# Kernel optimization log

Hardware: AMD Instinct MI355X
Metric: run time of the kernel (lower is better)

The kernel has to match this reference:

```python
import jax, jax.numpy as jnp
import numpy as np

NUM_JOINT = 19
BATCH = 262144
ROOT_SCALE = 200.0
# Topologically-ordered humanoid skeleton: parent[j] < j for all non-root joints.
# 0: hips, 1-4: spine/head chain, 5-8: left arm, 9-12: right arm, 13-15: left leg, 16-18: right leg
PARENTS = np.array([-1, 0, 1, 2, 3, 2, 5, 6, 7, 2, 9, 10, 11, 0, 13, 14, 0, 16, 17], dtype=np.int32)


def quaternion_to_matrix(q):
    # q: [..., 4] in (w, x, y, z) order (pytorch3d convention, non-unit tolerant)
    w, x, y, z = q[..., 0], q[..., 1], q[..., 2], q[..., 3]
    two_s = 2.0 / jnp.sum(q * q, axis=-1)
    r = jnp.stack([
        1.0 - two_s * (y * y + z * z), two_s * (x * y - z * w), two_s * (x * z + y * w),
        two_s * (x * y + z * w), 1.0 - two_s * (x * x + z * z), two_s * (y * z - x * w),
        two_s * (x * z - y * w), two_s * (y * z + x * w), 1.0 - two_s * (x * x + y * y),
    ], axis=-1)
    return r.reshape(q.shape[:-1] + (3, 3))


def setup_inputs() -> dict:
    key = jax.random.key(0)
    k1, k2, k3 = jax.random.split(key, 3)
    root_position = jax.random.normal(k1, (BATCH, 3), dtype=jnp.float32)
    joint = jax.random.normal(k2, (BATCH, NUM_JOINT * 4), dtype=jnp.float32)
    # Homogeneous translation matrices per bone: identity rotation, translation in column 3.
    trans = jax.random.normal(k3, (NUM_JOINT, 3), dtype=jnp.float32) * 10.0
    offsets = jnp.tile(jnp.eye(4, dtype=jnp.float32)[None], (NUM_JOINT, 1, 1))
    offsets = offsets.at[:, :3, 3].set(trans)
    return {"root_position": root_position, "joint": joint, "offsets": offsets}


def reference(root_position, joint, offsets):
    B = joint.shape[0]
    q = joint.reshape(B, NUM_JOINT, 4)
    R3 = quaternion_to_matrix(q)  # [B, J, 3, 3]
    R4 = jnp.zeros((B, NUM_JOINT, 4, 4), dtype=joint.dtype)
    R4 = R4.at[:, :, :3, :3].set(R3).at[:, :, 3, 3].set(1.0)
    # RT = rotation @ bone offset, batched over all joints at once
    RT = jnp.einsum('bjik,jkl->bjil', R4, offsets)  # [B, J, 4, 4]
    # Sequential parent-child chain over the (small, fixed) skeleton tree
    mats = [RT[:, 0]]
    for j in range(1, NUM_JOINT):
        mats.append(jnp.matmul(mats[PARENTS[j]], RT[:, j]))
    M = jnp.stack(mats, axis=1)  # [B, J, 4, 4] world transforms
    # joint position = column 3 of the homogeneous transform (== transpose row 3 in source)
    pos = M[:, :, :, 3]  # [B, J, 4]
    pos = pos.at[:, :, :3].add((root_position * ROOT_SCALE)[:, None, :])
    return pos
```

## Files before the change

kernel.cpp:

```cpp
#include <hip/hip_runtime.h>
#include <stdint.h>

#define NJ 19
#define ROOT_SCALE 200.0f
#define BLOCK 64
#define ROWF 76
#define ROWV 19

struct Xform { float r[9]; float t[3]; };

__device__ __forceinline__ void quat_rt(float w, float x, float y, float z,
                                        float tx, float ty, float tz, Xform& o) {
    float ts = 2.0f / (w*w + x*x + y*y + z*z);
    o.r[0] = 1.0f - ts*(y*y + z*z); o.r[1] = ts*(x*y - z*w);        o.r[2] = ts*(x*z + y*w);
    o.r[3] = ts*(x*y + z*w);        o.r[4] = 1.0f - ts*(x*x + z*z); o.r[5] = ts*(y*z - x*w);
    o.r[6] = ts*(x*z - y*w);        o.r[7] = ts*(y*z + x*w);        o.r[8] = 1.0f - ts*(x*x + y*y);
    o.t[0] = o.r[0]*tx + o.r[1]*ty + o.r[2]*tz;
    o.t[1] = o.r[3]*tx + o.r[4]*ty + o.r[5]*tz;
    o.t[2] = o.r[6]*tx + o.r[7]*ty + o.r[8]*tz;
}

__device__ __forceinline__ void compose(const Xform& p, const Xform& l, Xform& o) {
#pragma unroll
    for (int i = 0; i < 3; ++i) {
        o.r[i*3+0] = p.r[i*3+0]*l.r[0] + p.r[i*3+1]*l.r[3] + p.r[i*3+2]*l.r[6];
        o.r[i*3+1] = p.r[i*3+0]*l.r[1] + p.r[i*3+1]*l.r[4] + p.r[i*3+2]*l.r[7];
        o.r[i*3+2] = p.r[i*3+0]*l.r[2] + p.r[i*3+1]*l.r[5] + p.r[i*3+2]*l.r[8];
        o.t[i]     = p.r[i*3+0]*l.t[0] + p.r[i*3+1]*l.t[1] + p.r[i*3+2]*l.t[2] + p.t[i];
    }
}

__global__ __launch_bounds__(BLOCK, 2) void fk_kernel(
    const float* __restrict__ root, const float* __restrict__ joint,
    const float* __restrict__ offs, float* __restrict__ out, int batch)
{
    __shared__ float s[BLOCK * ROWF];
    const int tid = threadIdx.x;
    const int rowBase = blockIdx.x * BLOCK;
    const long long gbase = (long long)rowBase * ROWF;
    const int nvalid = min(BLOCK, batch - rowBase);

    if (nvalid == BLOCK) {
#pragma unroll
        for (int i = 0; i < ROWV; ++i) {
            __builtin_amdgcn_global_load_lds(
                (const __attribute__((address_space(1))) uint32_t*)
                    (joint + gbase + (long long)(i * BLOCK + tid) * 4),
                (__attribute__((address_space(3))) uint32_t*)(s + i * BLOCK * 4),
                16, 0, 0);
        }
    } else {
        for (int v = tid; v < nvalid * ROWV; v += BLOCK) {
            *(float4*)(s + 4 * v) =
                *(const float4*)(joint + gbase + (long long)v * 4);
        }
    }
    __syncthreads();

    if (tid < nvalid) {
        float* row = s + tid * ROWF;
        const int b = rowBase + tid;
        const float rx = root[(long long)b*3 + 0] * ROOT_SCALE;
        const float ry = root[(long long)b*3 + 1] * ROOT_SCALE;
        const float rz = root[(long long)b*3 + 2] * ROOT_SCALE;

        Xform cur, sv0, sv2, loc;
#pragma unroll
        for (int j = 0; j < NJ; ++j) {
            float4 q = *(const float4*)(&row[j*4]);
            float tx = offs[j*16 + 3], ty = offs[j*16 + 7], tz = offs[j*16 + 11];
            quat_rt(q.x, q.y, q.z, q.w, tx, ty, tz, loc);
            if (j == 0) {
                cur = loc;
            } else {
                Xform nxt;
                if (j == 5 || j == 9)        compose(sv2, loc, nxt);
                else if (j == 13 || j == 16) compose(sv0, loc, nxt);
                else                         compose(cur, loc, nxt);
                cur = nxt;
            }
            if (j == 0) sv0 = cur;
            if (j == 2) sv2 = cur;
            float4 o;
            o.x = cur.t[0] + rx;
            o.y = cur.t[1] + ry;
            o.z = cur.t[2] + rz;
            o.w = 1.0f;
            *(float4*)(&row[j*4]) = o;
        }
    }
    __syncthreads();

    if (nvalid == BLOCK) {
#pragma unroll
        for (int i = 0; i < ROWV; ++i) {
            int v = i * BLOCK + tid;
            *(float4*)(out + gbase + (long long)v * 4) = *(const float4*)(s + 4 * v);
        }
    } else {
        for (int v = tid; v < nvalid * ROWV; v += BLOCK) {
            *(float4*)(out + gbase + (long long)v * 4) = *(const float4*)(s + 4 * v);
        }
    }
}

extern "C" void kernel_launch(void* const* d_in, const int* in_sizes, int n_in,
                              void* d_out, int out_size, void* d_ws, size_t ws_size,
                              hipStream_t stream) {
    const float* root  = (const float*)d_in[0];
    const float* joint = (const float*)d_in[1];
    const float* offs  = (const float*)d_in[2];
    float* out = (float*)d_out;
    const int batch = in_sizes[1] / ROWF;
    const int grid = (batch + BLOCK - 1) / BLOCK;
    fk_kernel<<<grid, BLOCK, 0, stream>>>(root, joint, offs, out, batch);
}
```

Baseline: 151.1 us.

## Drop LDS staging and load quaternions per thread directly into registers

Removes the shared-memory staging of joint rows (global_load_lds plus barriers) and the LDS write-back. Each thread now loads its 19 float4 quaternions straight from global memory into registers and writes outputs directly. Block size grows from 64 to 256 with a different occupancy hint. Each thread reads a strided 304-byte row, so global accesses are no longer coalesced across the wavefront, and register pressure rises from holding all 19 quaternions.

```diff
diff --git a/kernel.cpp b/kernel.cpp
--- a/kernel.cpp
+++ b/kernel.cpp
@@ -1,11 +1,8 @@
 #include <hip/hip_runtime.h>
-#include <stdint.h>
 
 #define NJ 19
 #define ROOT_SCALE 200.0f
-#define BLOCK 64
-#define ROWF 76
-#define ROWV 19
+#define BLOCK 256
 
 struct Xform { float r[9]; float t[3]; };
 
@@ -30,77 +27,47 @@
     }
 }
 
-__global__ __launch_bounds__(BLOCK, 2) void fk_kernel(
+__global__ __launch_bounds__(BLOCK, 3) void fk_kernel(
     const float* __restrict__ root, const float* __restrict__ joint,
     const float* __restrict__ offs, float* __restrict__ out, int batch)
 {
-    __shared__ float s[BLOCK * ROWF];
-    const int tid = threadIdx.x;
-    const int rowBase = blockIdx.x * BLOCK;
-    const long long gbase = (long long)rowBase * ROWF;
-    const int nvalid = min(BLOCK, batch - rowBase);
+    const int b = blockIdx.x * BLOCK + threadIdx.x;
+    if (b >= batch) return;
 
-    if (nvalid == BLOCK) {
+    const float4* __restrict__ jq = (const float4*)joint;
+    float4* __restrict__ o4 = (float4*)out;
+    const long long base = (long long)b * NJ;
+
+    float4 q[NJ];
 #pragma unroll
-        for (int i = 0; i < ROWV; ++i) {
-            __builtin_amdgcn_global_load_lds(
-                (const __attribute__((address_space(1))) uint32_t*)
-                    (joint + gbase + (long long)(i * BLOCK + tid) * 4),
-                (__attribute__((address_space(3))) uint32_t*)(s + i * BLOCK * 4),
-                16, 0, 0);
+    for (int j = 0; j < NJ; ++j) q[j] = jq[base + j];
+
+    const float rx = root[(long long)b*3 + 0] * ROOT_SCALE;
+    const float ry = root[(long long)b*3 + 1] * ROOT_SCALE;
+    const float rz = root[(long long)b*3 + 2] * ROOT_SCALE;
+
+    Xform cur, sv0, sv2, loc;
+#pragma unroll
+    for (int j = 0; j < NJ; ++j) {
+        float tx = offs[j*16 + 3], ty = offs[j*16 + 7], tz = offs[j*16 + 11];
+        quat_rt(q[j].x, q[j].y, q[j].z, q[j].w, tx, ty, tz, loc);
+        if (j == 0) {
+            cur = loc;
+        } else {
+            Xform nxt;
+            if (j == 5 || j == 9)        compose(sv2, loc, nxt);
+            else if (j == 13 || j == 16) compose(sv0, loc, nxt);
+            else                         compose(cur, loc, nxt);
+            cur = nxt;
         }
-    } else {
-        for (int v = tid; v < nvalid * ROWV; v += BLOCK) {
-            *(float4*)(s + 4 * v) =
-                *(const float4*)(joint + gbase + (long long)v * 4);
-        }
-    }
-    __syncthreads();
-
-    if (tid < nvalid) {
-        float* row = s + tid * ROWF;
-        const int b = rowBase + tid;
-        const float rx = root[(long long)b*3 + 0] * ROOT_SCALE;
-        const float ry = root[(long long)b*3 + 1] * ROOT_SCALE;
-        const float rz = root[(long long)b*3 + 2] * ROOT_SCALE;
-
-        Xform cur, sv0, sv2, loc;
-#pragma unroll
-        for (int j = 0; j < NJ; ++j) {
-            float4 q = *(const float4*)(&row[j*4]);
-            float tx = offs[j*16 + 3], ty = offs[j*16 + 7], tz = offs[j*16 + 11];
-            quat_rt(q.x, q.y, q.z, q.w, tx, ty, tz, loc);
-            if (j == 0) {
-                cur = loc;
-            } else {
-                Xform nxt;
-                if (j == 5 || j == 9)        compose(sv2, loc, nxt);
-                else if (j == 13 || j == 16) compose(sv0, loc, nxt);
-                else                         compose(cur, loc, nxt);
-                cur = nxt;
-            }
-            if (j == 0) sv0 = cur;
-            if (j == 2) sv2 = cur;
-            float4 o;
-            o.x = cur.t[0] + rx;
-            o.y = cur.t[1] + ry;
-            o.z = cur.t[2] + rz;
-            o.w = 1.0f;
-            *(float4*)(&row[j*4]) = o;
-        }
-    }
-    __syncthreads();
-
-    if (nvalid == BLOCK) {
-#pragma unroll
-        for (int i = 0; i < ROWV; ++i) {
-            int v = i * BLOCK + tid;
-            *(float4*)(out + gbase + (long long)v * 4) = *(const float4*)(s + 4 * v);
-        }
-    } else {
-        for (int v = tid; v < nvalid * ROWV; v += BLOCK) {
-            *(float4*)(out + gbase + (long long)v * 4) = *(const float4*)(s + 4 * v);
-        }
+        if (j == 0) sv0 = cur;
+        if (j == 2) sv2 = cur;
+        float4 o;
+        o.x = cur.t[0] + rx;
+        o.y = cur.t[1] + ry;
+        o.z = cur.t[2] + rz;
+        o.w = 1.0f;
+        o4[base + j] = o;
     }
 }
 
@@ -111,7 +78,7 @@
     const float* joint = (const float*)d_in[1];
     const float* offs  = (const float*)d_in[2];
     float* out = (float*)d_out;
-    const int batch = in_sizes[1] / ROWF;
+    const int batch = in_sizes[1] / (NJ * 4);
     const int grid = (batch + BLOCK - 1) / BLOCK;
     fk_kernel<<<grid, BLOCK, 0, stream>>>(root, joint, offs, out, batch);
 }
```

New measurement: 240.0 us. 58.8% more time.

## Make FK kernel persistent with double-buffered async LDS prefetch

Applied to the files above, without the earlier changes.

Replaces the one-block-per-64-rows launch with a persistent grid of up to 1024 single-wavefront blocks. Each block loops over slabs and prefetches the next slab's joint and root data into a second LDS buffer through global_load_lds, gated by manual vmcnt waits, so loads overlap with compute. Bone offsets are hoisted into registers once per block. A separate tail kernel handles leftover rows. The aim is to hide memory latency with only one wave per block. The cost is reliance on exact hand-counted vmcnt values and higher register use.

```diff
diff --git a/kernel.cpp b/kernel.cpp
--- a/kernel.cpp
+++ b/kernel.cpp
@@ -6,6 +6,11 @@
 #define BLOCK 64
 #define ROWF 76
 #define ROWV 19
+#define SLABF (BLOCK * ROWF)
+#define ROOTF (BLOCK * 3)
+
+typedef const __attribute__((address_space(1))) uint32_t* gptr_t;
+typedef __attribute__((address_space(3))) uint32_t* lptr_t;
 
 struct Xform { float r[9]; float t[3]; };
 
@@ -30,77 +35,126 @@
     }
 }
 
-__global__ __launch_bounds__(BLOCK, 2) void fk_kernel(
+__device__ __forceinline__ void issue_group(const float* __restrict__ joint,
+                                            const float* __restrict__ root,
+                                            long long slab, float* jb, float* rb, int tid) {
+#pragma unroll
+    for (int i = 0; i < ROWV; ++i) {
+        __builtin_amdgcn_global_load_lds(
+            (gptr_t)(joint + slab * SLABF + (long long)(i * BLOCK + tid) * 4),
+            (lptr_t)(jb + i * BLOCK * 4), 16, 0, 0);
+    }
+    if (tid < 48) {
+        __builtin_amdgcn_global_load_lds(
+            (gptr_t)(root + slab * ROOTF + tid * 4),
+            (lptr_t)rb, 16, 0, 0);
+    }
+}
+
+__global__ __launch_bounds__(BLOCK) void fk_pipe(
     const float* __restrict__ root, const float* __restrict__ joint,
-    const float* __restrict__ offs, float* __restrict__ out, int batch)
+    const float* __restrict__ offs, float* __restrict__ out, int nslab)
 {
-    __shared__ float s[BLOCK * ROWF];
+    __shared__ float jb[2][SLABF];
+    __shared__ float rb[2][ROOTF];
     const int tid = threadIdx.x;
-    const int rowBase = blockIdx.x * BLOCK;
-    const long long gbase = (long long)rowBase * ROWF;
-    const int nvalid = min(BLOCK, batch - rowBase);
 
-    if (nvalid == BLOCK) {
+    float tx[NJ], ty[NJ], tz[NJ];
 #pragma unroll
-        for (int i = 0; i < ROWV; ++i) {
-            __builtin_amdgcn_global_load_lds(
-                (const __attribute__((address_space(1))) uint32_t*)
-                    (joint + gbase + (long long)(i * BLOCK + tid) * 4),
-                (__attribute__((address_space(3))) uint32_t*)(s + i * BLOCK * 4),
-                16, 0, 0);
+    for (int j = 0; j < NJ; ++j) {
+        tx[j] = offs[j*16 + 3]; ty[j] = offs[j*16 + 7]; tz[j] = offs[j*16 + 11];
+    }
+    asm volatile("s_waitcnt vmcnt(0)" ::: "memory");
+
+    long long slab = blockIdx.x;
+    const int stride = gridDim.x;
+    if (slab >= nslab) return;
+
+    int p = 0;
+    issue_group(joint, root, slab, jb[0], rb[0], tid);
+
+    bool first = true;
+    for (; slab < nslab; slab += stride) {
+        const bool has_next = (slab + stride < (long long)nslab);
+        if (has_next)
+            issue_group(joint, root, slab + stride, jb[p^1], rb[p^1], tid);
+
+        if (first) { if (has_next) asm volatile("s_waitcnt vmcnt(20)" ::: "memory");
+                     else          asm volatile("s_waitcnt vmcnt(0)"  ::: "memory"); }
+        else       { if (has_next) asm volatile("s_waitcnt vmcnt(39)" ::: "memory");
+                     else          asm volatile("s_waitcnt vmcnt(19)" ::: "memory"); }
+        first = false;
+
+        {
+            float* row = &jb[p][tid * ROWF];
+            const float rx = rb[p][tid*3 + 0] * ROOT_SCALE;
+            const float ry = rb[p][tid*3 + 1] * ROOT_SCALE;
+            const float rz = rb[p][tid*3 + 2] * ROOT_SCALE;
+
+            Xform cur, sv0, sv2, loc;
+#pragma unroll
+            for (int j = 0; j < NJ; ++j) {
+                float4 q = *(const float4*)(&row[j*4]);
+                quat_rt(q.x, q.y, q.z, q.w, tx[j], ty[j], tz[j], loc);
+                if (j == 0) {
+                    cur = loc;
+                } else {
+                    Xform nxt;
+                    if (j == 5 || j == 9)        compose(sv2, loc, nxt);
+                    else if (j == 13 || j == 16) compose(sv0, loc, nxt);
+                    else                         compose(cur, loc, nxt);
+                    cur = nxt;
+                }
+                if (j == 0) sv0 = cur;
+                if (j == 2) sv2 = cur;
+                float4 o;
+                o.x = cur.t[0] + rx;
+                o.y = cur.t[1] + ry;
+                o.z = cur.t[2] + rz;
+                o.w = 1.0f;
+                *(float4*)(&row[j*4]) = o;
+            }
         }
-    } else {
-        for (int v = tid; v < nvalid * ROWV; v += BLOCK) {
-            *(float4*)(s + 4 * v) =
-                *(const float4*)(joint + gbase + (long long)v * 4);
+
+        {
+            const long long gb = slab * SLABF;
+#pragma unroll
+            for (int i = 0; i < ROWV; ++i) {
+                const int v = i * BLOCK + tid;
+                *(float4*)(out + gb + (long long)v * 4) = *(const float4*)(&jb[p][v*4]);
+            }
         }
+        p ^= 1;
     }
-    __syncthreads();
+}
 
-    if (tid < nvalid) {
-        float* row = s + tid * ROWF;
-        const int b = rowBase + tid;
-        const float rx = root[(long long)b*3 + 0] * ROOT_SCALE;
-        const float ry = root[(long long)b*3 + 1] * ROOT_SCALE;
-        const float rz = root[(long long)b*3 + 2] * ROOT_SCALE;
-
-        Xform cur, sv0, sv2, loc;
+__global__ void fk_tail(const float* __restrict__ root, const float* __restrict__ joint,
+                        const float* __restrict__ offs, float* __restrict__ out,
+                        int start, int batch)
+{
+    const int b = start + threadIdx.x;
+    if (b >= batch) return;
+    const long long base = (long long)b * ROWF;
+    const float rx = root[(long long)b*3 + 0] * ROOT_SCALE;
+    const float ry = root[(long long)b*3 + 1] * ROOT_SCALE;
+    const float rz = root[(long long)b*3 + 2] * ROOT_SCALE;
+    Xform cur, sv0, sv2, loc;
 #pragma unroll
-        for (int j = 0; j < NJ; ++j) {
-            float4 q = *(const float4*)(&row[j*4]);
-            float tx = offs[j*16 + 3], ty = offs[j*16 + 7], tz = offs[j*16 + 11];
-            quat_rt(q.x, q.y, q.z, q.w, tx, ty, tz, loc);
-            if (j == 0) {
-                cur = loc;
-            } else {
-                Xform nxt;
-                if (j == 5 || j == 9)        compose(sv2, loc, nxt);
-                else if (j == 13 || j == 16) compose(sv0, loc, nxt);
-                else                         compose(cur, loc, nxt);
-                cur = nxt;
-            }
-            if (j == 0) sv0 = cur;
-            if (j == 2) sv2 = cur;
-            float4 o;
-            o.x = cur.t[0] + rx;
-            o.y = cur.t[1] + ry;
-            o.z = cur.t[2] + rz;
-            o.w = 1.0f;
-            *(float4*)(&row[j*4]) = o;
+    for (int j = 0; j < NJ; ++j) {
+        float4 q = *(const float4*)(joint + base + j*4);
+        quat_rt(q.x, q.y, q.z, q.w, offs[j*16+3], offs[j*16+7], offs[j*16+11], loc);
+        if (j == 0) cur = loc;
+        else {
+            Xform nxt;
+            if (j == 5 || j == 9)        compose(sv2, loc, nxt);
+            else if (j == 13 || j == 16) compose(sv0, loc, nxt);
+            else                         compose(cur, loc, nxt);
+            cur = nxt;
         }
-    }
-    __syncthreads();
-
-    if (nvalid == BLOCK) {
-#pragma unroll
-        for (int i = 0; i < ROWV; ++i) {
-            int v = i * BLOCK + tid;
-            *(float4*)(out + gbase + (long long)v * 4) = *(const float4*)(s + 4 * v);
-        }
-    } else {
-        for (int v = tid; v < nvalid * ROWV; v += BLOCK) {
-            *(float4*)(out + gbase + (long long)v * 4) = *(const float4*)(s + 4 * v);
-        }
+        if (j == 0) sv0 = cur;
+        if (j == 2) sv2 = cur;
+        float4 o; o.x = cur.t[0]+rx; o.y = cur.t[1]+ry; o.z = cur.t[2]+rz; o.w = 1.0f;
+        *(float4*)(out + base + j*4) = o;
     }
 }
 
@@ -112,6 +166,13 @@
     const float* offs  = (const float*)d_in[2];
     float* out = (float*)d_out;
     const int batch = in_sizes[1] / ROWF;
-    const int grid = (batch + BLOCK - 1) / BLOCK;
-    fk_kernel<<<grid, BLOCK, 0, stream>>>(root, joint, offs, out, batch);
+    const int nslab = batch / BLOCK;
+    const int tail  = batch - nslab * BLOCK;
+    if (nslab > 0) {
+        const int grid = nslab < 1024 ? nslab : 1024;
+        fk_pipe<<<grid, BLOCK, 0, stream>>>(root, joint, offs, out, nslab);
+    }
+    if (tail > 0) {
+        fk_tail<<<1, BLOCK, 0, stream>>>(root, joint, offs, out, nslab * BLOCK, batch);
+    }
 }
```

Result: slower. 157.0 us (+3.9%).
